# Kernel tuning notes

Hardware: AMD Instinct MI355X
Metric: run time of the kernel (lower is better)

The kernel has to match this reference:

```python
import jax, jax.numpy as jnp
import numpy as np

M, K, N = 32, 8192, 8192      # tokens, infeatures, outfeatures
GROUP = 128                   # quantization group size along K
PACK = 8                      # 32 bits / 4 bits per value


def _dequant(qweight, scales):
    """Unpack int4 nibbles (packed 8-per-int32 along K) and apply per-group
    symmetric dequant: w = (q - 8) * scale, matching Marlin's fused dequant."""
    kp, n = qweight.shape  # (K//8, N)
    shifts = (4 * jnp.arange(PACK, dtype=jnp.int32))[None, :, None]
    q = ((qweight[:, None, :] >> shifts) & 15)          # (K//8, 8, N)
    q = q.reshape(kp * PACK, n).astype(jnp.float32)     # (K, N)
    groups = scales.shape[0]
    gsz = (kp * PACK) // groups
    w = (q.reshape(groups, gsz, n) - 8.0) * scales[:, None, :]
    return w.reshape(kp * PACK, n)                      # (K, N) fp


def setup_inputs() -> dict:
    key = jax.random.key(0)
    kA, kQ, kS, kB = jax.random.split(key, 4)
    A = jax.random.normal(kA, (M, K), jnp.float32)
    # draw raw 4-bit codes then pack 8 of them into each int32 along K
    q4 = jax.random.randint(kQ, (K, N), 0, 16, jnp.int32)
    shifts = (4 * jnp.arange(PACK, dtype=jnp.int32))[None, :, None]
    qweight = jnp.sum(q4.reshape(K // PACK, PACK, N) << shifts, axis=1).astype(jnp.int32)
    scales = jax.random.uniform(kS, (K // GROUP, N), jnp.float32, 0.005, 0.02)
    bias = jax.random.normal(kB, (N,), jnp.float32) * 0.01
    return {"A": A, "qweight": qweight, "scales": scales, "bias": bias}


def reference(A, qweight, scales, bias):
    # Marlin mul(A, B, C, s) computes C = A @ dequant(B, s); then + bias
    W = _dequant(qweight, scales)          # (K, N)
    return A @ W + bias                    # (M, N)
```

## Files before the change

### kernel.cpp

```cpp
#include <hip/hip_runtime.h>
#include <hip/hip_bf16.h>
#include <stdint.h>

#define M_DIM 32
#define K_DIM 8192
#define N_DIM 8192
#define NGROUPS 64
#define KSPLIT 8
#define KPART (K_DIM / KSPLIT)
#define GPART (NGROUPS / KSPLIT)
#define BN 64
#define NPH 4

#define QSTRIDE 72
#define ASTRIDE 132

typedef __attribute__((ext_vector_type(8))) short short8;
typedef __attribute__((ext_vector_type(4))) float floatx4;

__global__ void marlin_prep_kernel(const float* __restrict__ A,
                                   uint16_t* __restrict__ Abf,
                                   float* __restrict__ R) {
    const int m = blockIdx.x;
    const int qtr = blockIdx.y;
    const int t = threadIdx.x;
    const int octet = qtr * 256 + t;
    const int k0 = octet * 8;

    const float* a = A + m * K_DIM + k0;
    uint16_t b[8];
    float sum = 0.f;
#pragma unroll
    for (int j = 0; j < 8; j++) {
        union { __hip_bfloat16 h; uint16_t u; } cv;
        cv.h = __float2bfloat16(a[j]);
        b[j] = cv.u;
        sum += __bfloat162float(cv.h);
    }
    uint32_t w0 = (uint32_t)b[0] | ((uint32_t)b[4] << 16);
    uint32_t w1 = (uint32_t)b[1] | ((uint32_t)b[5] << 16);
    uint32_t w2 = (uint32_t)b[2] | ((uint32_t)b[6] << 16);
    uint32_t w3 = (uint32_t)b[3] | ((uint32_t)b[7] << 16);
    *(uint4*)(Abf + (size_t)m * K_DIM + k0) = make_uint4(w0, w1, w2, w3);

#pragma unroll
    for (int off = 1; off < 16; off <<= 1) sum += __shfl_xor(sum, off, 16);
    if ((t & 15) == 0) R[m * NGROUPS + qtr * 16 + (t >> 4)] = sum;
}

__global__ __launch_bounds__(512, 4) void
MarlinQuantLinear_68556267979256_kernel(const int* __restrict__ qw,
                                        const float* __restrict__ scales,
                                        const uint16_t* __restrict__ Abf,
                                        const float* __restrict__ R,
                                        float* __restrict__ parts) {
    __shared__ uint32_t qbuf[2][32 * QSTRIDE];
    __shared__ uint32_t abuf[2][32 * ASTRIDE];
    __shared__ float    r_lds[32 * 9];

    const int bx = blockIdx.x;
    const int bz = blockIdx.y;
    const int nbase = bx * BN;
    const int gbase = bz * GPART;

    const int tid = threadIdx.x;
    const int w = tid >> 6;
    const int lane = tid & 63;
    const int quad = lane >> 4;
    const int l16 = lane & 15;
    const int mtile = w & 1;
    const int ntile = w >> 1;
    const int ncol = nbase + ntile * 16 + l16;

    const int sr = tid >> 4;
    const int sc = (tid & 15) * 4;
    const int ac = (tid & 15) * 8;
    const int* qsrc = qw + (size_t)(bz * 128 + sr) * N_DIM + nbase + sc;
    const uint32_t* asrc = (const uint32_t*)Abf + (size_t)sr * (K_DIM / 2)
                           + bz * (KPART / 2) + ac;

    uint4 qst = *(const uint4*)qsrc;
    uint4 a0  = *(const uint4*)asrc;
    uint4 a1  = *(const uint4*)(asrc + 4);

    const float* scol = scales + (size_t)gbase * N_DIM + ncol;
    float s[GPART];
#pragma unroll
    for (int g = 0; g < GPART; g++) s[g] = scol[g * N_DIM];

    if (tid < 256) {
        const int mm = tid >> 3, gg = tid & 7;
        r_lds[mm * 9 + gg] = 136.0f * R[mm * NGROUPS + gbase + gg];
    }

    floatx4 C = {0.f, 0.f, 0.f, 0.f};

#pragma unroll
    for (int p = 0; p < NPH; p++) {
        *(uint4*)&qbuf[p & 1][sr * QSTRIDE + sc] = qst;
        *(uint4*)&abuf[p & 1][sr * ASTRIDE + ac] = a0;
        *(uint4*)&abuf[p & 1][sr * ASTRIDE + ac + 4] = a1;
        asm volatile("s_waitcnt lgkmcnt(0)" ::: "memory");
        __builtin_amdgcn_s_barrier();

        if (p + 1 < NPH) {
            qst = *(const uint4*)(qsrc + (size_t)(p + 1) * 32 * N_DIM);
            a0  = *(const uint4*)(asrc + (p + 1) * 128);
            a1  = *(const uint4*)(asrc + (p + 1) * 128 + 4);
        }

#pragma unroll
        for (int gg = 0; gg < 2; gg++) {
            floatx4 accg = {0.f, 0.f, 0.f, 0.f};
#pragma unroll
            for (int t = 0; t < 4; t++) {
                const uint32_t q =
                    qbuf[p & 1][(gg * 16 + t * 4 + quad) * QSTRIDE + ntile * 16 + l16];
                union { uint32_t u[4]; short8 v; } fb;
                fb.u[0] = ( q        & 0x000F000Fu) | 0x43004300u;
                fb.u[1] = ((q >> 4)  & 0x000F000Fu) | 0x43004300u;
                fb.u[2] = ((q >> 8)  & 0x000F000Fu) | 0x43004300u;
                fb.u[3] = ((q >> 12) & 0x000F000Fu) | 0x43004300u;
                const short8 fa = *(const short8*)
                    &abuf[p & 1][(mtile * 16 + l16) * ASTRIDE + gg * 64 + t * 16 + quad * 4];
                accg = __builtin_amdgcn_mfma_f32_16x16x32_bf16(fa, fb.v, accg, 0, 0, 0);
            }
            const int g = p * 2 + gg;
#pragma unroll
            for (int r = 0; r < 4; r++) {
                const float tval = accg[r] - r_lds[(mtile * 16 + quad * 4 + r) * 9 + g];
                C[r] = fmaf(s[g], tval, C[r]);
            }
        }
    }

    float* pp = parts + ((size_t)bz * M_DIM + mtile * 16 + quad * 4) * N_DIM + ncol;
#pragma unroll
    for (int r = 0; r < 4; r++) pp[r * N_DIM] = C[r];
}

__global__ __launch_bounds__(256) void
marlin_reduce_kernel(const float* __restrict__ parts,
                     const float* __restrict__ bias,
                     float* __restrict__ out) {
    const int idx = blockIdx.x * 256 + threadIdx.x;
    const int c4 = idx & (N_DIM / 4 - 1);
    const float4* p4 = (const float4*)parts;
    float4 acc = *(const float4*)(bias + c4 * 4);
#pragma unroll
    for (int bz = 0; bz < KSPLIT; bz++) {
        const float4 v = p4[(size_t)bz * (M_DIM * N_DIM / 4) + idx];
        acc.x += v.x; acc.y += v.y; acc.z += v.z; acc.w += v.w;
    }
    ((float4*)out)[idx] = acc;
}

extern "C" void kernel_launch(void* const* d_in, const int* in_sizes, int n_in,
                              void* d_out, int out_size, void* d_ws, size_t ws_size,
                              hipStream_t stream) {
    const float* A      = (const float*)d_in[0];
    const int*   qw     = (const int*)d_in[1];
    const float* scales = (const float*)d_in[2];
    const float* bias   = (const float*)d_in[3];
    float* out = (float*)d_out;

    uint16_t* Abf   = (uint16_t*)d_ws;
    float*    R     = (float*)((char*)d_ws + (size_t)M_DIM * K_DIM * 2);
    float*    parts = (float*)((char*)d_ws + (1 << 20));

    marlin_prep_kernel<<<dim3(M_DIM, 4), 256, 0, stream>>>(A, Abf, R);
    MarlinQuantLinear_68556267979256_kernel<<<dim3(N_DIM / BN, KSPLIT), 512, 0, stream>>>(
        qw, scales, Abf, R, parts);
    marlin_reduce_kernel<<<dim3((M_DIM * N_DIM / 4) / 256), 256, 0, stream>>>(
        parts, bias, out);
}
```

Measured before the change: 93.96 us.

## Widen N tile to 256 with per-group pipeline and LDS-staged scales

Each block now covers 256 output columns instead of 64, and each wave computes four 16-column MFMA tiles that reuse one A fragment load. The K loop runs per quantization group (8 stages of 16 packed rows) instead of 4 phases. Scales are staged through LDS, and the grid is transposed so K-split blocks for the same N tile are adjacent. This cuts redundant A reads and improves reuse, but there are four times fewer blocks (256), occupancy is lowered to 2 blocks per SM and more barriers are needed.

```diff
diff --git a/kernel.cpp b/kernel.cpp
--- a/kernel.cpp
+++ b/kernel.cpp
@@ -9,11 +9,11 @@
 #define KSPLIT 8
 #define KPART (K_DIM / KSPLIT)
 #define GPART (NGROUPS / KSPLIT)
-#define BN 64
-#define NPH 4
+#define BN 256
 
-#define QSTRIDE 72
-#define ASTRIDE 132
+#define QSTRIDE 264
+#define ASTRIDE 68
+#define SSTRIDE 260
 
 typedef __attribute__((ext_vector_type(8))) short short8;
 typedef __attribute__((ext_vector_type(4))) float floatx4;
@@ -48,18 +48,19 @@
     if ((t & 15) == 0) R[m * NGROUPS + qtr * 16 + (t >> 4)] = sum;
 }
 
-__global__ __launch_bounds__(512, 4) void
+__global__ __launch_bounds__(512, 2) void
 MarlinQuantLinear_68556267979256_kernel(const int* __restrict__ qw,
                                         const float* __restrict__ scales,
                                         const uint16_t* __restrict__ Abf,
                                         const float* __restrict__ R,
                                         float* __restrict__ parts) {
-    __shared__ uint32_t qbuf[2][32 * QSTRIDE];
+    __shared__ uint32_t qbuf[2][16 * QSTRIDE];
     __shared__ uint32_t abuf[2][32 * ASTRIDE];
+    __shared__ float    s_lds[GPART * SSTRIDE];
     __shared__ float    r_lds[32 * 9];
 
-    const int bx = blockIdx.x;
-    const int bz = blockIdx.y;
+    const int bz = blockIdx.x;
+    const int bx = blockIdx.y;
     const int nbase = bx * BN;
     const int gbase = bz * GPART;
 
@@ -70,73 +71,83 @@
     const int l16 = lane & 15;
     const int mtile = w & 1;
     const int ntile = w >> 1;
-    const int ncol = nbase + ntile * 16 + l16;
 
-    const int sr = tid >> 4;
-    const int sc = (tid & 15) * 4;
-    const int ac = (tid & 15) * 8;
-    const int* qsrc = qw + (size_t)(bz * 128 + sr) * N_DIM + nbase + sc;
-    const uint32_t* asrc = (const uint32_t*)Abf + (size_t)sr * (K_DIM / 2)
+    const int qr = tid >> 5;
+    const int qc = (tid & 31) * 4;
+    const int* qsrc = qw + (size_t)(bz * 128 + qr) * N_DIM + nbase + qc;
+    const int ar = tid >> 4;
+    const int ac = (tid & 15) * 4;
+    const uint32_t* asrc = (const uint32_t*)Abf + (size_t)ar * (K_DIM / 2)
                            + bz * (KPART / 2) + ac;
 
-    uint4 qst = *(const uint4*)qsrc;
-    uint4 a0  = *(const uint4*)asrc;
-    uint4 a1  = *(const uint4*)(asrc + 4);
+    uint4 q0 = *(const uint4*)qsrc;
+    uint4 q1 = *(const uint4*)(qsrc + 128);
+    uint4 a0 = *(const uint4*)asrc;
 
-    const float* scol = scales + (size_t)gbase * N_DIM + ncol;
-    float s[GPART];
-#pragma unroll
-    for (int g = 0; g < GPART; g++) s[g] = scol[g * N_DIM];
-
+    {
+        const int sg = tid >> 6, scc = (tid & 63) * 4;
+        const float4 sv = *(const float4*)(scales + (size_t)(gbase + sg) * N_DIM
+                                           + nbase + scc);
+        *(float4*)&s_lds[sg * SSTRIDE + scc] = sv;
+    }
     if (tid < 256) {
         const int mm = tid >> 3, gg = tid & 7;
         r_lds[mm * 9 + gg] = 136.0f * R[mm * NGROUPS + gbase + gg];
     }
 
-    floatx4 C = {0.f, 0.f, 0.f, 0.f};
+    floatx4 C[4] = {{0.f, 0.f, 0.f, 0.f}, {0.f, 0.f, 0.f, 0.f},
+                    {0.f, 0.f, 0.f, 0.f}, {0.f, 0.f, 0.f, 0.f}};
 
 #pragma unroll
-    for (int p = 0; p < NPH; p++) {
-        *(uint4*)&qbuf[p & 1][sr * QSTRIDE + sc] = qst;
-        *(uint4*)&abuf[p & 1][sr * ASTRIDE + ac] = a0;
-        *(uint4*)&abuf[p & 1][sr * ASTRIDE + ac + 4] = a1;
+    for (int g = 0; g < GPART; g++) {
+        *(uint4*)&qbuf[g & 1][qr * QSTRIDE + qc] = q0;
+        *(uint4*)&qbuf[g & 1][qr * QSTRIDE + qc + 128] = q1;
+        *(uint4*)&abuf[g & 1][ar * ASTRIDE + ac] = a0;
         asm volatile("s_waitcnt lgkmcnt(0)" ::: "memory");
         __builtin_amdgcn_s_barrier();
 
-        if (p + 1 < NPH) {
-            qst = *(const uint4*)(qsrc + (size_t)(p + 1) * 32 * N_DIM);
-            a0  = *(const uint4*)(asrc + (p + 1) * 128);
-            a1  = *(const uint4*)(asrc + (p + 1) * 128 + 4);
+        if (g + 1 < GPART) {
+            q0 = *(const uint4*)(qsrc + (size_t)(g + 1) * 16 * N_DIM);
+            q1 = *(const uint4*)(qsrc + (size_t)(g + 1) * 16 * N_DIM + 128);
+            a0 = *(const uint4*)(asrc + (g + 1) * 64);
         }
 
+        floatx4 accg[4] = {{0.f, 0.f, 0.f, 0.f}, {0.f, 0.f, 0.f, 0.f},
+                           {0.f, 0.f, 0.f, 0.f}, {0.f, 0.f, 0.f, 0.f}};
 #pragma unroll
-        for (int gg = 0; gg < 2; gg++) {
-            floatx4 accg = {0.f, 0.f, 0.f, 0.f};
+        for (int t = 0; t < 4; t++) {
+            const short8 fa = *(const short8*)
+                &abuf[g & 1][(mtile * 16 + l16) * ASTRIDE + t * 16 + quad * 4];
 #pragma unroll
-            for (int t = 0; t < 4; t++) {
+            for (int f = 0; f < 4; f++) {
                 const uint32_t q =
-                    qbuf[p & 1][(gg * 16 + t * 4 + quad) * QSTRIDE + ntile * 16 + l16];
+                    qbuf[g & 1][(t * 4 + quad) * QSTRIDE + ntile * 64 + f * 16 + l16];
                 union { uint32_t u[4]; short8 v; } fb;
                 fb.u[0] = ( q        & 0x000F000Fu) | 0x43004300u;
                 fb.u[1] = ((q >> 4)  & 0x000F000Fu) | 0x43004300u;
                 fb.u[2] = ((q >> 8)  & 0x000F000Fu) | 0x43004300u;
                 fb.u[3] = ((q >> 12) & 0x000F000Fu) | 0x43004300u;
-                const short8 fa = *(const short8*)
-                    &abuf[p & 1][(mtile * 16 + l16) * ASTRIDE + gg * 64 + t * 16 + quad * 4];
-                accg = __builtin_amdgcn_mfma_f32_16x16x32_bf16(fa, fb.v, accg, 0, 0, 0);
+                accg[f] = __builtin_amdgcn_mfma_f32_16x16x32_bf16(fa, fb.v, accg[f], 0, 0, 0);
             }
-            const int g = p * 2 + gg;
+        }
+#pragma unroll
+        for (int f = 0; f < 4; f++) {
+            const float sv = s_lds[g * SSTRIDE + ntile * 64 + f * 16 + l16];
 #pragma unroll
             for (int r = 0; r < 4; r++) {
-                const float tval = accg[r] - r_lds[(mtile * 16 + quad * 4 + r) * 9 + g];
-                C[r] = fmaf(s[g], tval, C[r]);
+                const float tval = accg[f][r] - r_lds[(mtile * 16 + quad * 4 + r) * 9 + g];
+                C[f][r] = fmaf(sv, tval, C[f][r]);
             }
         }
     }
 
-    float* pp = parts + ((size_t)bz * M_DIM + mtile * 16 + quad * 4) * N_DIM + ncol;
 #pragma unroll
-    for (int r = 0; r < 4; r++) pp[r * N_DIM] = C[r];
+    for (int f = 0; f < 4; f++) {
+        const int ncol = nbase + ntile * 64 + f * 16 + l16;
+        float* pp = parts + ((size_t)bz * M_DIM + mtile * 16 + quad * 4) * N_DIM + ncol;
+#pragma unroll
+        for (int r = 0; r < 4; r++) pp[r * N_DIM] = C[f][r];
+    }
 }
 
 __global__ __launch_bounds__(256) void
@@ -169,7 +180,7 @@
     float*    parts = (float*)((char*)d_ws + (1 << 20));
 
     marlin_prep_kernel<<<dim3(M_DIM, 4), 256, 0, stream>>>(A, Abf, R);
-    MarlinQuantLinear_68556267979256_kernel<<<dim3(N_DIM / BN, KSPLIT), 512, 0, stream>>>(
+    MarlinQuantLinear_68556267979256_kernel<<<dim3(KSPLIT, N_DIM / BN), 512, 0, stream>>>(
         qw, scales, Abf, R, parts);
     marlin_reduce_kernel<<<dim3((M_DIM * N_DIM / 4) / 256), 256, 0, stream>>>(
         parts, bias, out);
```

New measurement: 91.39 us, median of 2. 2.7% less time.
